# Performance work log

Measured on AMD Instinct MI355X. Metric: run time of the kernel, lower is better.

Reference implementation:

```python
import jax, jax.numpy as jnp
import numpy as np

EPS = 1e-5

def _layernorm(x, g, b):
    m = jnp.mean(x, axis=-1, keepdims=True)
    v = jnp.var(x, axis=-1, keepdims=True)
    return (x - m) * jax.lax.rsqrt(v + EPS) * g + b

def setup_inputs() -> dict:
    key = jax.random.key(0)
    ks = jax.random.split(key, 8)
    B, N, D, H = 4, 2048, 1024, 16
    F = 2 * D
    s = 0.02
    return {
        "x": jax.random.normal(ks[0], (B, N, D), jnp.float32),
        "mask": jnp.zeros((B, N, N), jnp.float32),
        "Wq": jax.random.normal(ks[1], (D, D), jnp.float32) * s,
        "Wk": jax.random.normal(ks[2], (D, D), jnp.float32) * s,
        "Wv": jax.random.normal(ks[3], (D, D), jnp.float32) * s,
        "Wc": jax.random.normal(ks[4], (D, D), jnp.float32) * s,
        "bc": jnp.zeros((D,), jnp.float32),
        "W1": jax.random.normal(ks[5], (D, F), jnp.float32) * s,
        "b1": jnp.zeros((F,), jnp.float32),
        "W2": jax.random.normal(ks[6], (F, D), jnp.float32) * s,
        "b2": jnp.zeros((D,), jnp.float32),
        "g1": jnp.ones((D,), jnp.float32),
        "be1": jnp.zeros((D,), jnp.float32),
        "g2": jnp.ones((D,), jnp.float32),
        "be2": jnp.zeros((D,), jnp.float32),
    }

def reference(x, mask, Wq, Wk, Wv, Wc, bc, W1, b1, W2, b2, g1, be1, g2, be2):
    B, N, D = x.shape
    H = 16
    Dh = D // H
    scale = 1.0 / np.sqrt(Dh).astype(np.float32)
    # projections -> [B, H, N, Dh]
    def heads(t):
        return t.reshape(B, N, H, Dh).transpose(0, 2, 1, 3)
    q = heads(x @ Wq)
    k = heads(x @ Wk)
    v = heads(x @ Wv)
    score = jnp.einsum('bhnd,bhmd->bhnm', q, k) * scale + mask[:, None, :, :]
    attn = jnp.einsum('bhnm,bhmd->bhnd', jax.nn.softmax(score, axis=-1), v)
    attn = attn.transpose(0, 2, 1, 3).reshape(B, N, D)
    x = x + attn @ Wc + bc
    x = _layernorm(x, g1, be1)
    x = x + jnp.maximum(x @ W1 + b1, 0.0) @ W2 + b2
    x = _layernorm(x, g2, be2)
    return x
```

## Files before the change

### kernel.cpp

```cpp
#include <hip/hip_runtime.h>
#include <hip/hip_bf16.h>


#define DEV __device__ __forceinline__

using s16x8 = __attribute__((ext_vector_type(8))) short;
using f32x4 = __attribute__((ext_vector_type(4))) float;

DEV unsigned short f2bf(float f) {
  unsigned u = __float_as_uint(f);
  u += 0x7fffu + ((u >> 16) & 1u);
  return (unsigned short)(u >> 16);
}
DEV unsigned pack2bf(float a, float b) {
  return (unsigned)f2bf(a) | ((unsigned)f2bf(b) << 16);
}
DEV unsigned cvt_pk_bf16(float lo, float hi) {
  unsigned r;
  asm("v_cvt_pk_bf16_f32 %0, %1, %2" : "=v"(r) : "v"(lo), "v"(hi));
  return r;
}

typedef __attribute__((address_space(3))) unsigned lds_u32_t;
typedef const __attribute__((address_space(1))) unsigned glb_u32_t;

DEV void gld_lds16(const void* g, void* l) {
  __builtin_amdgcn_global_load_lds((glb_u32_t*)g, (lds_u32_t*)l, 16, 0, 0);
}

template<int RELU, int RESID, int OUTF>
__global__ __launch_bounds__(256)
void gemm_bt(const unsigned short* __restrict__ A, const unsigned short* __restrict__ Bt,
             unsigned short* __restrict__ Cb, float* __restrict__ Cf,
             const float* __restrict__ bias, const float* __restrict__ resid,
             int M, int N, int K)
{
  __shared__ unsigned short As[128 * 32];
  __shared__ unsigned short Bs[128 * 32];
  const int tid  = threadIdx.x;
  const int wave = tid >> 6, lane = tid & 63;
  const int g = lane >> 4, q = lane & 15;

  const int nwg  = gridDim.x * gridDim.y;
  const int flat = blockIdx.y * gridDim.x + blockIdx.x;
  const int rm   = (nwg & 7) ? flat : ((flat & 7) * (nwg >> 3) + (flat >> 3));
  const int m0 = (rm / gridDim.x) * 128, n0 = (rm % gridDim.x) * 128;
  const int wr = wave >> 1, wc = wave & 1;

  f32x4 acc[4][4] = {};

  const int i0 = wave * 512 + lane * 8;
  const int i1 = 2048 + i0;

  for (int kt = 0; kt < K; kt += 32) {
    gld_lds16(A  + (size_t)(m0 + (i0 >> 5)) * K + kt + (i0 & 31), As + wave * 512);
    gld_lds16(Bt + (size_t)(n0 + (i0 >> 5)) * K + kt + (i0 & 31), Bs + wave * 512);
    gld_lds16(A  + (size_t)(m0 + (i1 >> 5)) * K + kt + (i1 & 31), As + 2048 + wave * 512);
    gld_lds16(Bt + (size_t)(n0 + (i1 >> 5)) * K + kt + (i1 & 31), Bs + 2048 + wave * 512);
    __syncthreads();
    s16x8 a[4], b[4];
#pragma unroll
    for (int m = 0; m < 4; ++m)
      a[m] = *(const s16x8*)(As + (wr * 64 + m * 16 + q) * 32 + g * 8);
#pragma unroll
    for (int n = 0; n < 4; ++n)
      b[n] = *(const s16x8*)(Bs + (wc * 64 + n * 16 + q) * 32 + g * 8);
#pragma unroll
    for (int m = 0; m < 4; ++m)
#pragma unroll
      for (int n = 0; n < 4; ++n)
        acc[m][n] = __builtin_amdgcn_mfma_f32_16x16x32_bf16(a[m], b[n], acc[m][n], 0, 0, 0);
    __syncthreads();
  }

#pragma unroll
  for (int n = 0; n < 4; ++n) {
    const int col = n0 + wc * 64 + n * 16 + q;
    const float bv = bias ? bias[col] : 0.0f;
#pragma unroll
    for (int m = 0; m < 4; ++m) {
      const int row0 = m0 + wr * 64 + m * 16 + g * 4;
#pragma unroll
      for (int r = 0; r < 4; ++r) {
        float v = acc[m][n][r] + bv;
        if (RELU) v = fmaxf(v, 0.0f);
        if (RESID) v += resid[(size_t)(row0 + r) * N + col];
        if (OUTF) Cf[(size_t)(row0 + r) * N + col] = v;
        else      Cb[(size_t)(row0 + r) * N + col] = f2bf(v);
      }
    }
  }
}

__global__ __launch_bounds__(256, 4)
void attn_kernel(const unsigned short* __restrict__ qkv,
                 const unsigned short* __restrict__ vt,
                 const float* __restrict__ mask,
                 unsigned short* __restrict__ outb)
{
  __shared__ unsigned short Ks[2][4096];
  __shared__ unsigned short Vs[2][4096];
  __shared__ unsigned short Pl[4][1024];
  const int tid = threadIdx.x, wave = tid >> 6, lane = tid & 63;
  const int g = lane >> 4, q = lane & 15;

  const int flat = blockIdx.y * 32 + blockIdx.x;
  const int rm   = (flat & 7) * 256 + (flat >> 3);
  const int qt = rm & 31, bh = rm >> 5;
  const int b = bh >> 4, h = bh & 15;
  const int qrow = qt * 64 + wave * 16;
  const size_t tok0 = (size_t)b * 2048;

  const unsigned short* Qp = qkv + (tok0 + qrow + q) * 3072 + h * 64;
  const s16x8 bq0 = *(const s16x8*)(Qp + g * 8);
  const s16x8 bq1 = *(const s16x8*)(Qp + 32 + g * 8);
  const float* Mp = mask + ((size_t)b * 2048 + qrow + q) * 2048;

  const int lr = lane >> 3;
  const int sc = (lane & 7) ^ lr;
  const unsigned short* Kg = qkv + tok0 * 3072 + 1024 + h * 64
                           + (size_t)(wave * 16 + lr) * 3072 + sc * 8;
  const unsigned short* Vg = vt + ((size_t)bh * 64 + wave * 16 + lr) * 2048 + sc * 8;
  unsigned short* KsW = Ks[0] + wave * 1024;
  unsigned short* VsW = Vs[0] + wave * 1024;

  auto STAGE = [&](int buf, int t) {
    const size_t ko = (size_t)t * (64 * 3072);
    const int    vo = t * 64;
    gld_lds16(Kg + ko,            KsW + buf * 4096);
    gld_lds16(Kg + ko + 8 * 3072, KsW + buf * 4096 + 512);
    gld_lds16(Vg + vo,            VsW + buf * 4096);
    gld_lds16(Vg + vo + 8 * 2048, VsW + buf * 4096 + 512);
  };

  f32x4 ot[4] = {};
  f32x4 mkc[4], mkn[4];
  float mrun = -3.0e38f, lsum = 0.0f;
  char* Pw = (char*)&Pl[wave][0];

  STAGE(0, 0);
#pragma unroll
  for (int m2 = 0; m2 < 4; ++m2) mkc[m2] = *(const f32x4*)(Mp + m2 * 16 + g * 4);
  __syncthreads();

  int cur = 0;
  for (int t = 0; t < 32; ++t) {
    if (t < 31) {
      STAGE(cur ^ 1, t + 1);
#pragma unroll
      for (int m2 = 0; m2 < 4; ++m2)
        mkn[m2] = *(const f32x4*)(Mp + (t + 1) * 64 + m2 * 16 + g * 4);
    }
    const unsigned short* Kt = Ks[cur];
    const unsigned short* Vt = Vs[cur];

    f32x4 st[4] = {};
    __builtin_amdgcn_s_setprio(1);
#pragma unroll
    for (int m2 = 0; m2 < 4; ++m2) {
      const unsigned short* kp = Kt + (m2 * 16 + q) * 64;
      const s16x8 ak0 = *(const s16x8*)(kp + ((g       ^ (q & 7)) * 8));
      const s16x8 ak1 = *(const s16x8*)(kp + (((g + 4) ^ (q & 7)) * 8));
      st[m2] = __builtin_amdgcn_mfma_f32_16x16x32_bf16(ak0, bq0, st[m2], 0, 0, 0);
      st[m2] = __builtin_amdgcn_mfma_f32_16x16x32_bf16(ak1, bq1, st[m2], 0, 0, 0);
    }
    __builtin_amdgcn_s_setprio(0);

    float tmax = -3.0e38f;
#pragma unroll
    for (int m2 = 0; m2 < 4; ++m2) {
#pragma unroll
      for (int r = 0; r < 4; ++r) {
        st[m2][r] = st[m2][r] * 0.125f + mkc[m2][r];
        tmax = fmaxf(tmax, st[m2][r]);
      }
    }
    tmax = fmaxf(tmax, __shfl_xor(tmax, 16));
    tmax = fmaxf(tmax, __shfl_xor(tmax, 32));
    const float mnew  = fmaxf(mrun, tmax);
    const float alpha = __expf(mrun - mnew);
    mrun = mnew;

    float rsum = 0.0f;
#pragma unroll
    for (int m2 = 0; m2 < 4; ++m2) {
#pragma unroll
      for (int r = 0; r < 4; ++r) {
        st[m2][r] = __expf(st[m2][r] - mnew);
        rsum += st[m2][r];
      }
      const int bir  = m2 * 32 + g * 8;
      const int addr = q * 128 + ((((bir >> 4) ^ (q & 7))) << 4) + (bir & 15);
      uint2 pk;
      pk.x = cvt_pk_bf16(st[m2][0], st[m2][1]);
      pk.y = cvt_pk_bf16(st[m2][2], st[m2][3]);
      *(uint2*)(Pw + addr) = pk;
    }
    rsum += __shfl_xor(rsum, 16);
    rsum += __shfl_xor(rsum, 32);
    lsum = lsum * alpha + rsum;
#pragma unroll
    for (int m = 0; m < 4; ++m) {
      ot[m][0] *= alpha; ot[m][1] *= alpha; ot[m][2] *= alpha; ot[m][3] *= alpha;
    }

    __builtin_amdgcn_s_setprio(1);
#pragma unroll
    for (int kb = 0; kb < 2; ++kb) {
      const int blk = (kb * 4 + g) ^ (q & 7);
      const s16x8 pb = *(const s16x8*)(Pw + q * 128 + blk * 16);
#pragma unroll
      for (int m = 0; m < 4; ++m) {
        const s16x8 av = *(const s16x8*)(Vt + (m * 16 + q) * 64 + blk * 8);
        ot[m] = __builtin_amdgcn_mfma_f32_16x16x32_bf16(av, pb, ot[m], 0, 0, 0);
      }
    }
    __builtin_amdgcn_s_setprio(0);

#pragma unroll
    for (int m2 = 0; m2 < 4; ++m2) mkc[m2] = mkn[m2];
    __syncthreads();
    cur ^= 1;
  }

  const float inv = 1.0f / lsum;
#pragma unroll
  for (int m = 0; m < 4; ++m) {
    const int bir  = m * 32 + g * 8;
    const int addr = q * 128 + (((bir >> 4) ^ (q & 7)) << 4) + (bir & 15);
    uint2 pk;
    pk.x = cvt_pk_bf16(ot[m][0] * inv, ot[m][1] * inv);
    pk.y = cvt_pk_bf16(ot[m][2] * inv, ot[m][3] * inv);
    *(uint2*)(Pw + addr) = pk;
  }
#pragma unroll
  for (int p = 0; p < 2; ++p) {
    const int c  = p * 64 + lane;
    const int qq = c >> 3, cc = c & 7;
    const int blk = cc ^ (qq & 7);
    const s16x8 vv = *(const s16x8*)(Pw + qq * 128 + blk * 16);
    *(s16x8*)(outb + (tok0 + qrow + qq) * 1024 + h * 64 + cc * 8) = vv;
  }
}

__global__ __launch_bounds__(256)
void ln_kernel(const float* __restrict__ in, float* __restrict__ outf,
               unsigned short* __restrict__ outb,
               const float* __restrict__ gam, const float* __restrict__ bet)
{
  __shared__ float red[8];
  const int row = blockIdx.x, tid = threadIdx.x;
  const f32x4 v = *(const f32x4*)(in + (size_t)row * 1024 + tid * 4);
  float s  = v[0] + v[1] + v[2] + v[3];
  float ss = v[0]*v[0] + v[1]*v[1] + v[2]*v[2] + v[3]*v[3];
#pragma unroll
  for (int o = 1; o < 64; o <<= 1) { s += __shfl_xor(s, o); ss += __shfl_xor(ss, o); }
  if ((tid & 63) == 0) { red[tid >> 6] = s; red[4 + (tid >> 6)] = ss; }
  __syncthreads();
  s  = red[0] + red[1] + red[2] + red[3];
  ss = red[4] + red[5] + red[6] + red[7];
  const float mean = s * (1.0f / 1024.0f);
  const float var  = ss * (1.0f / 1024.0f) - mean * mean;
  const float rstd = rsqrtf(var + 1e-5f);
  const f32x4 gm = *(const f32x4*)(gam + tid * 4);
  const f32x4 bt = *(const f32x4*)(bet + tid * 4);
  f32x4 o;
#pragma unroll
  for (int j = 0; j < 4; ++j) o[j] = (v[j] - mean) * rstd * gm[j] + bt[j];
  if (outf) *(f32x4*)(outf + (size_t)row * 1024 + tid * 4) = o;
  if (outb) {
    uint2 pk; pk.x = pack2bf(o[0], o[1]); pk.y = pack2bf(o[2], o[3]);
    *(uint2*)(outb + (size_t)row * 1024 + tid * 4) = pk;
  }
}

__global__ __launch_bounds__(256)
void tcast_kernel(const float* __restrict__ in, unsigned short* __restrict__ out, int R, int C)
{
  __shared__ float t[32][33];
  const int tx = threadIdx.x & 31, ty = threadIdx.x >> 5;
  const int c0 = blockIdx.x * 32, r0 = blockIdx.y * 32;
#pragma unroll
  for (int k = 0; k < 4; ++k)
    t[ty + k * 8][tx] = in[(size_t)(r0 + ty + k * 8) * C + c0 + tx];
  __syncthreads();
#pragma unroll
  for (int k = 0; k < 4; ++k)
    out[(size_t)(c0 + ty + k * 8) * R + r0 + tx] = f2bf(t[tx][ty + k * 8]);
}

__global__ __launch_bounds__(256)
void tv_kernel(const unsigned short* __restrict__ qkv, unsigned short* __restrict__ vt)
{
  __shared__ unsigned short t[32][33];
  const int tx = threadIdx.x & 31, ty = threadIdx.x >> 5;
  const int c0 = blockIdx.x * 32, r0 = blockIdx.y * 32, b = blockIdx.z;
  const unsigned short* in = qkv + (size_t)b * 2048 * 3072 + 2048;
  unsigned short* out = vt + (size_t)b * 1024 * 2048;
#pragma unroll
  for (int k = 0; k < 4; ++k)
    t[ty + k * 8][tx] = in[(size_t)(r0 + ty + k * 8) * 3072 + c0 + tx];
  __syncthreads();
#pragma unroll
  for (int k = 0; k < 4; ++k)
    out[(size_t)(c0 + ty + k * 8) * 2048 + r0 + tx] = t[tx][ty + k * 8];
}

__global__ __launch_bounds__(256)
void cast_x_kernel(const float* __restrict__ in, unsigned short* __restrict__ out)
{
  const size_t i = ((size_t)blockIdx.x * 256 + threadIdx.x) * 4;
  const f32x4 v = *(const f32x4*)(in + i);
  uint2 pk; pk.x = pack2bf(v[0], v[1]); pk.y = pack2bf(v[2], v[3]);
  *(uint2*)(out + i) = pk;
}

extern "C" void kernel_launch(void* const* d_in, const int* in_sizes, int n_in,
                              void* d_out, int out_size, void* d_ws, size_t ws_size,
                              hipStream_t stream)
{
  (void)in_sizes; (void)n_in; (void)out_size; (void)ws_size;
  const float* x   = (const float*)d_in[0];
  const float* msk = (const float*)d_in[1];
  const float* Wq  = (const float*)d_in[2];
  const float* Wk  = (const float*)d_in[3];
  const float* Wv  = (const float*)d_in[4];
  const float* Wc  = (const float*)d_in[5];
  const float* bc  = (const float*)d_in[6];
  const float* W1  = (const float*)d_in[7];
  const float* b1  = (const float*)d_in[8];
  const float* W2  = (const float*)d_in[9];
  const float* b2  = (const float*)d_in[10];
  const float* g1  = (const float*)d_in[11];
  const float* be1 = (const float*)d_in[12];
  const float* g2  = (const float*)d_in[13];
  const float* be2 = (const float*)d_in[14];
  float* out = (float*)d_out;
  char* ws = (char*)d_ws;
  const size_t MB = 1u << 20;
  unsigned short* xb    = (unsigned short*)(ws + 0 * MB);
  unsigned short* wqkvt = (unsigned short*)(ws + 16 * MB);
  unsigned short* wct   = (unsigned short*)(ws + 22 * MB);
  unsigned short* w1t   = (unsigned short*)(ws + 24 * MB);
  unsigned short* w2t   = (unsigned short*)(ws + 28 * MB);
  unsigned short* qkv   = (unsigned short*)(ws + 32 * MB);
  unsigned short* vt    = (unsigned short*)(ws + 80 * MB);
  unsigned short* attnb = xb;
  float*          y1    = (float*)(ws + 32 * MB);
  unsigned short* h1b   = (unsigned short*)(ws + 64 * MB);
  float*          h1f   = (float*)(ws + 96 * MB);
  unsigned short* midb  = (unsigned short*)(ws + 128 * MB);

  cast_x_kernel<<<8192, 256, 0, stream>>>(x, xb);
  tcast_kernel<<<dim3(32, 32), 256, 0, stream>>>(Wq, wqkvt,               1024, 1024);
  tcast_kernel<<<dim3(32, 32), 256, 0, stream>>>(Wk, wqkvt + 1024 * 1024, 1024, 1024);
  tcast_kernel<<<dim3(32, 32), 256, 0, stream>>>(Wv, wqkvt + 2048 * 1024, 1024, 1024);
  tcast_kernel<<<dim3(32, 32), 256, 0, stream>>>(Wc, wct,                 1024, 1024);
  tcast_kernel<<<dim3(64, 32), 256, 0, stream>>>(W1, w1t,                 1024, 2048);
  tcast_kernel<<<dim3(32, 64), 256, 0, stream>>>(W2, w2t,                 2048, 1024);

  gemm_bt<0, 0, 0><<<dim3(24, 64), 256, 0, stream>>>(xb, wqkvt, qkv, nullptr,
                                                     nullptr, nullptr, 8192, 3072, 1024);
  tv_kernel<<<dim3(32, 64, 4), 256, 0, stream>>>(qkv, vt);
  attn_kernel<<<dim3(32, 64), 256, 0, stream>>>(qkv, vt, msk, attnb);
  gemm_bt<0, 1, 1><<<dim3(8, 64), 256, 0, stream>>>(attnb, wct, nullptr, y1,
                                                    bc, x, 8192, 1024, 1024);
  ln_kernel<<<8192, 256, 0, stream>>>(y1, h1f, h1b, g1, be1);
  gemm_bt<1, 0, 0><<<dim3(16, 64), 256, 0, stream>>>(h1b, w1t, midb, nullptr,
                                                     b1, nullptr, 8192, 2048, 1024);
  gemm_bt<0, 1, 1><<<dim3(8, 64), 256, 0, stream>>>(midb, w2t, nullptr, out,
                                                    b2, h1f, 8192, 1024, 2048);
  ln_kernel<<<8192, 256, 0, stream>>>(out, out, nullptr, g2, be2);
}
```

Baseline: 470.6 us.

## Fuse V transpose into QKV GEMM and double attention query rows per wave

The QKV GEMM epilogue now writes the V columns directly in transposed layout, so the separate tv_kernel launch and its extra pass over V go away. The attention kernel processes 32 query rows per wave (128 per block), so each K/V tile staged in LDS is reused twice as often. Grid size is halved and occupancy is lowered to 3 blocks. Softmax switches to exp2 with a lazy rescale that only updates the running max when the new max exceeds it by more than 8. Mask prefetch across iterations is dropped in favour of in-iteration loads, and register pressure rises.

```diff
diff --git a/kernel.cpp b/kernel.cpp
--- a/kernel.cpp
+++ b/kernel.cpp
@@ -20,6 +20,12 @@
   asm("v_cvt_pk_bf16_f32 %0, %1, %2" : "=v"(r) : "v"(lo), "v"(hi));
   return r;
 }
+DEV f32x4 vmax4(f32x4 a, f32x4 b) {
+  f32x4 r;
+  r[0] = fmaxf(a[0], b[0]); r[1] = fmaxf(a[1], b[1]);
+  r[2] = fmaxf(a[2], b[2]); r[3] = fmaxf(a[3], b[3]);
+  return r;
+}
 
 typedef __attribute__((address_space(3))) unsigned lds_u32_t;
 typedef const __attribute__((address_space(1))) unsigned glb_u32_t;
@@ -28,11 +34,12 @@
   __builtin_amdgcn_global_load_lds((glb_u32_t*)g, (lds_u32_t*)l, 16, 0, 0);
 }
 
-template<int RELU, int RESID, int OUTF>
+template<int RELU, int RESID, int OUTF, int VOUT>
 __global__ __launch_bounds__(256)
 void gemm_bt(const unsigned short* __restrict__ A, const unsigned short* __restrict__ Bt,
              unsigned short* __restrict__ Cb, float* __restrict__ Cf,
              const float* __restrict__ bias, const float* __restrict__ resid,
+             unsigned short* __restrict__ vtout,
              int M, int N, int K)
 {
   __shared__ unsigned short As[128 * 32];
@@ -76,23 +83,36 @@
 #pragma unroll
   for (int n = 0; n < 4; ++n) {
     const int col = n0 + wc * 64 + n * 16 + q;
-    const float bv = bias ? bias[col] : 0.0f;
-#pragma unroll
-    for (int m = 0; m < 4; ++m) {
-      const int row0 = m0 + wr * 64 + m * 16 + g * 4;
-#pragma unroll
-      for (int r = 0; r < 4; ++r) {
-        float v = acc[m][n][r] + bv;
-        if (RELU) v = fmaxf(v, 0.0f);
-        if (RESID) v += resid[(size_t)(row0 + r) * N + col];
-        if (OUTF) Cf[(size_t)(row0 + r) * N + col] = v;
-        else      Cb[(size_t)(row0 + r) * N + col] = f2bf(v);
+    if (VOUT && col >= 2048) {
+      const int cv = col - 2048;
+#pragma unroll
+      for (int m = 0; m < 4; ++m) {
+        const int row0 = m0 + wr * 64 + m * 16 + g * 4;
+        const int bb = row0 >> 11;
+        ushort4 pk;
+        pk.x = f2bf(acc[m][n][0]); pk.y = f2bf(acc[m][n][1]);
+        pk.z = f2bf(acc[m][n][2]); pk.w = f2bf(acc[m][n][3]);
+        *(ushort4*)(vtout + ((size_t)bb * 1024 + cv) * 2048 + (row0 & 2047)) = pk;
       }
-    }
-  }
-}
-
-__global__ __launch_bounds__(256, 4)
+    } else {
+      const float bv = bias ? bias[col] : 0.0f;
+#pragma unroll
+      for (int m = 0; m < 4; ++m) {
+        const int row0 = m0 + wr * 64 + m * 16 + g * 4;
+#pragma unroll
+        for (int r = 0; r < 4; ++r) {
+          float v = acc[m][n][r] + bv;
+          if (RELU) v = fmaxf(v, 0.0f);
+          if (RESID) v += resid[(size_t)(row0 + r) * N + col];
+          if (OUTF) Cf[(size_t)(row0 + r) * N + col] = v;
+          else      Cb[(size_t)(row0 + r) * N + col] = f2bf(v);
+        }
+      }
+    }
+  }
+}
+
+__global__ __launch_bounds__(256, 3)
 void attn_kernel(const unsigned short* __restrict__ qkv,
                  const unsigned short* __restrict__ vt,
                  const float* __restrict__ mask,
@@ -100,21 +120,26 @@
 {
   __shared__ unsigned short Ks[2][4096];
   __shared__ unsigned short Vs[2][4096];
-  __shared__ unsigned short Pl[4][1024];
+  __shared__ unsigned short Pl[4][2048];
   const int tid = threadIdx.x, wave = tid >> 6, lane = tid & 63;
   const int g = lane >> 4, q = lane & 15;
 
-  const int flat = blockIdx.y * 32 + blockIdx.x;
-  const int rm   = (flat & 7) * 256 + (flat >> 3);
-  const int qt = rm & 31, bh = rm >> 5;
+  const int flat = blockIdx.y * 16 + blockIdx.x;
+  const int rm   = (flat & 7) * 128 + (flat >> 3);
+  const int qt = rm & 15, bh = rm >> 4;
   const int b = bh >> 4, h = bh & 15;
-  const int qrow = qt * 64 + wave * 16;
+  const int qrow = qt * 128 + wave * 32;
   const size_t tok0 = (size_t)b * 2048;
 
-  const unsigned short* Qp = qkv + (tok0 + qrow + q) * 3072 + h * 64;
-  const s16x8 bq0 = *(const s16x8*)(Qp + g * 8);
-  const s16x8 bq1 = *(const s16x8*)(Qp + 32 + g * 8);
-  const float* Mp = mask + ((size_t)b * 2048 + qrow + q) * 2048;
+  s16x8 bq[2][2];
+#pragma unroll
+  for (int qb = 0; qb < 2; ++qb) {
+    const unsigned short* Qp = qkv + (tok0 + qrow + qb * 16 + q) * 3072 + h * 64;
+    bq[qb][0] = *(const s16x8*)(Qp + g * 8);
+    bq[qb][1] = *(const s16x8*)(Qp + 32 + g * 8);
+  }
+  const float* Mp0 = mask + ((size_t)b * 2048 + qrow + q) * 2048;
+  const float* Mp1 = Mp0 + 16 * 2048;
 
   const int lr = lane >> 3;
   const int sc = (lane & 7) ^ lr;
@@ -133,108 +158,132 @@
     gld_lds16(Vg + vo + 8 * 2048, VsW + buf * 4096 + 512);
   };
 
-  f32x4 ot[4] = {};
-  f32x4 mkc[4], mkn[4];
-  float mrun = -3.0e38f, lsum = 0.0f;
+  f32x4 ot[2][4] = {};
+  float mrun0 = -3.0e38f, mrun1 = -3.0e38f;
+  float mnl0 = 0.0f, mnl1 = 0.0f;
+  float lsum0 = 0.0f, lsum1 = 0.0f;
   char* Pw = (char*)&Pl[wave][0];
+  const float SC  = 0.125f;
+  const float L2E = 1.4426950408889634f;
 
   STAGE(0, 0);
-#pragma unroll
-  for (int m2 = 0; m2 < 4; ++m2) mkc[m2] = *(const f32x4*)(Mp + m2 * 16 + g * 4);
   __syncthreads();
 
   int cur = 0;
+#pragma unroll 1
   for (int t = 0; t < 32; ++t) {
-    if (t < 31) {
-      STAGE(cur ^ 1, t + 1);
-#pragma unroll
-      for (int m2 = 0; m2 < 4; ++m2)
-        mkn[m2] = *(const f32x4*)(Mp + (t + 1) * 64 + m2 * 16 + g * 4);
+    if (t < 31) STAGE(cur ^ 1, t + 1);
+    f32x4 mk0[4], mk1[4];
+#pragma unroll
+    for (int m2 = 0; m2 < 4; ++m2) {
+      mk0[m2] = *(const f32x4*)(Mp0 + t * 64 + m2 * 16 + g * 4);
+      mk1[m2] = *(const f32x4*)(Mp1 + t * 64 + m2 * 16 + g * 4);
     }
     const unsigned short* Kt = Ks[cur];
     const unsigned short* Vt = Vs[cur];
 
-    f32x4 st[4] = {};
+    f32x4 st0[4] = {}, st1[4] = {};
     __builtin_amdgcn_s_setprio(1);
 #pragma unroll
     for (int m2 = 0; m2 < 4; ++m2) {
       const unsigned short* kp = Kt + (m2 * 16 + q) * 64;
       const s16x8 ak0 = *(const s16x8*)(kp + ((g       ^ (q & 7)) * 8));
       const s16x8 ak1 = *(const s16x8*)(kp + (((g + 4) ^ (q & 7)) * 8));
-      st[m2] = __builtin_amdgcn_mfma_f32_16x16x32_bf16(ak0, bq0, st[m2], 0, 0, 0);
-      st[m2] = __builtin_amdgcn_mfma_f32_16x16x32_bf16(ak1, bq1, st[m2], 0, 0, 0);
+      st0[m2] = __builtin_amdgcn_mfma_f32_16x16x32_bf16(ak0, bq[0][0], st0[m2], 0, 0, 0);
+      st1[m2] = __builtin_amdgcn_mfma_f32_16x16x32_bf16(ak0, bq[1][0], st1[m2], 0, 0, 0);
+      st0[m2] = __builtin_amdgcn_mfma_f32_16x16x32_bf16(ak1, bq[0][1], st0[m2], 0, 0, 0);
+      st1[m2] = __builtin_amdgcn_mfma_f32_16x16x32_bf16(ak1, bq[1][1], st1[m2], 0, 0, 0);
     }
     __builtin_amdgcn_s_setprio(0);
 
-    float tmax = -3.0e38f;
 #pragma unroll
     for (int m2 = 0; m2 < 4; ++m2) {
 #pragma unroll
       for (int r = 0; r < 4; ++r) {
-        st[m2][r] = st[m2][r] * 0.125f + mkc[m2][r];
-        tmax = fmaxf(tmax, st[m2][r]);
+        st0[m2][r] = fmaf(st0[m2][r], SC, mk0[m2][r]);
+        st1[m2][r] = fmaf(st1[m2][r], SC, mk1[m2][r]);
       }
     }
-    tmax = fmaxf(tmax, __shfl_xor(tmax, 16));
-    tmax = fmaxf(tmax, __shfl_xor(tmax, 32));
-    const float mnew  = fmaxf(mrun, tmax);
-    const float alpha = __expf(mrun - mnew);
-    mrun = mnew;
-
-    float rsum = 0.0f;
+    f32x4 a0 = vmax4(vmax4(st0[0], st0[1]), vmax4(st0[2], st0[3]));
+    f32x4 a1 = vmax4(vmax4(st1[0], st1[1]), vmax4(st1[2], st1[3]));
+    float t0 = fmaxf(fmaxf(a0[0], a0[1]), fmaxf(a0[2], a0[3]));
+    float t1 = fmaxf(fmaxf(a1[0], a1[1]), fmaxf(a1[2], a1[3]));
+    t0 = fmaxf(t0, __shfl_xor(t0, 16));
+    t0 = fmaxf(t0, __shfl_xor(t0, 32));
+    t1 = fmaxf(t1, __shfl_xor(t1, 16));
+    t1 = fmaxf(t1, __shfl_xor(t1, 32));
+
+    if (!__all(t0 <= mrun0 + 8.0f && t1 <= mrun1 + 8.0f)) {
+      const float mn0 = fmaxf(mrun0, t0), mn1 = fmaxf(mrun1, t1);
+      const float al0 = exp2f((mrun0 - mn0) * L2E);
+      const float al1 = exp2f((mrun1 - mn1) * L2E);
+      mrun0 = mn0; mrun1 = mn1;
+      mnl0 = mn0 * L2E; mnl1 = mn1 * L2E;
+      lsum0 *= al0; lsum1 *= al1;
+#pragma unroll
+      for (int m = 0; m < 4; ++m)
+#pragma unroll
+        for (int r = 0; r < 4; ++r) { ot[0][m][r] *= al0; ot[1][m][r] *= al1; }
+    }
+
+    float rs0 = 0.0f, rs1 = 0.0f;
 #pragma unroll
     for (int m2 = 0; m2 < 4; ++m2) {
 #pragma unroll
       for (int r = 0; r < 4; ++r) {
-        st[m2][r] = __expf(st[m2][r] - mnew);
-        rsum += st[m2][r];
+        st0[m2][r] = exp2f(fmaf(st0[m2][r], L2E, -mnl0));
+        st1[m2][r] = exp2f(fmaf(st1[m2][r], L2E, -mnl1));
       }
-      const int bir  = m2 * 32 + g * 8;
-      const int addr = q * 128 + ((((bir >> 4) ^ (q & 7))) << 4) + (bir & 15);
-      uint2 pk;
-      pk.x = cvt_pk_bf16(st[m2][0], st[m2][1]);
-      pk.y = cvt_pk_bf16(st[m2][2], st[m2][3]);
-      *(uint2*)(Pw + addr) = pk;
-    }
-    rsum += __shfl_xor(rsum, 16);
-    rsum += __shfl_xor(rsum, 32);
-    lsum = lsum * alpha + rsum;
-#pragma unroll
-    for (int m = 0; m < 4; ++m) {
-      ot[m][0] *= alpha; ot[m][1] *= alpha; ot[m][2] *= alpha; ot[m][3] *= alpha;
-    }
+      rs0 += (st0[m2][0] + st0[m2][1]) + (st0[m2][2] + st0[m2][3]);
+      rs1 += (st1[m2][0] + st1[m2][1]) + (st1[m2][2] + st1[m2][3]);
+      const int bir = m2 * 32 + g * 8;
+      const int ca  = (((bir >> 4) ^ (q & 7)) << 4) + (bir & 15);
+      uint2 pk0, pk1;
+      pk0.x = cvt_pk_bf16(st0[m2][0], st0[m2][1]);
+      pk0.y = cvt_pk_bf16(st0[m2][2], st0[m2][3]);
+      pk1.x = cvt_pk_bf16(st1[m2][0], st1[m2][1]);
+      pk1.y = cvt_pk_bf16(st1[m2][2], st1[m2][3]);
+      *(uint2*)(Pw + q * 128 + ca)        = pk0;
+      *(uint2*)(Pw + (16 + q) * 128 + ca) = pk1;
+    }
+    rs0 += __shfl_xor(rs0, 16); rs0 += __shfl_xor(rs0, 32);
+    rs1 += __shfl_xor(rs1, 16); rs1 += __shfl_xor(rs1, 32);
+    lsum0 += rs0; lsum1 += rs1;
 
     __builtin_amdgcn_s_setprio(1);
 #pragma unroll
     for (int kb = 0; kb < 2; ++kb) {
       const int blk = (kb * 4 + g) ^ (q & 7);
-      const s16x8 pb = *(const s16x8*)(Pw + q * 128 + blk * 16);
+      const s16x8 pb0 = *(const s16x8*)(Pw + q * 128 + blk * 16);
+      const s16x8 pb1 = *(const s16x8*)(Pw + (16 + q) * 128 + blk * 16);
 #pragma unroll
       for (int m = 0; m < 4; ++m) {
         const s16x8 av = *(const s16x8*)(Vt + (m * 16 + q) * 64 + blk * 8);
-        ot[m] = __builtin_amdgcn_mfma_f32_16x16x32_bf16(av, pb, ot[m], 0, 0, 0);
+        ot[0][m] = __builtin_amdgcn_mfma_f32_16x16x32_bf16(av, pb0, ot[0][m], 0, 0, 0);
+        ot[1][m] = __builtin_amdgcn_mfma_f32_16x16x32_bf16(av, pb1, ot[1][m], 0, 0, 0);
       }
     }
     __builtin_amdgcn_s_setprio(0);
 
-#pragma unroll
-    for (int m2 = 0; m2 < 4; ++m2) mkc[m2] = mkn[m2];
     __syncthreads();
     cur ^= 1;
   }
 
-  const float inv = 1.0f / lsum;
+  const float inv0 = 1.0f / lsum0, inv1 = 1.0f / lsum1;
 #pragma unroll
   for (int m = 0; m < 4; ++m) {
-    const int bir  = m * 32 + g * 8;
-    const int addr = q * 128 + (((bir >> 4) ^ (q & 7)) << 4) + (bir & 15);
-    uint2 pk;
-    pk.x = cvt_pk_bf16(ot[m][0] * inv, ot[m][1] * inv);
-    pk.y = cvt_pk_bf16(ot[m][2] * inv, ot[m][3] * inv);
-    *(uint2*)(Pw + addr) = pk;
-  }
-#pragma unroll
-  for (int p = 0; p < 2; ++p) {
+    const int bir = m * 32 + g * 8;
+    const int ca  = (((bir >> 4) ^ (q & 7)) << 4) + (bir & 15);
+    uint2 pk0, pk1;
+    pk0.x = cvt_pk_bf16(ot[0][m][0] * inv0, ot[0][m][1] * inv0);
+    pk0.y = cvt_pk_bf16(ot[0][m][2] * inv0, ot[0][m][3] * inv0);
+    pk1.x = cvt_pk_bf16(ot[1][m][0] * inv1, ot[1][m][1] * inv1);
+    pk1.y = cvt_pk_bf16(ot[1][m][2] * inv1, ot[1][m][3] * inv1);
+    *(uint2*)(Pw + q * 128 + ca)        = pk0;
+    *(uint2*)(Pw + (16 + q) * 128 + ca) = pk1;
+  }
+#pragma unroll
+  for (int p = 0; p < 4; ++p) {
     const int c  = p * 64 + lane;
     const int qq = c >> 3, cc = c & 7;
     const int blk = cc ^ (qq & 7);
@@ -287,23 +336,6 @@
 #pragma unroll
   for (int k = 0; k < 4; ++k)
     out[(size_t)(c0 + ty + k * 8) * R + r0 + tx] = f2bf(t[tx][ty + k * 8]);
-}
-
-__global__ __launch_bounds__(256)
-void tv_kernel(const unsigned short* __restrict__ qkv, unsigned short* __restrict__ vt)
-{
-  __shared__ unsigned short t[32][33];
-  const int tx = threadIdx.x & 31, ty = threadIdx.x >> 5;
-  const int c0 = blockIdx.x * 32, r0 = blockIdx.y * 32, b = blockIdx.z;
-  const unsigned short* in = qkv + (size_t)b * 2048 * 3072 + 2048;
-  unsigned short* out = vt + (size_t)b * 1024 * 2048;
-#pragma unroll
-  for (int k = 0; k < 4; ++k)
-    t[ty + k * 8][tx] = in[(size_t)(r0 + ty + k * 8) * 3072 + c0 + tx];
-  __syncthreads();
-#pragma unroll
-  for (int k = 0; k < 4; ++k)
-    out[(size_t)(c0 + ty + k * 8) * 2048 + r0 + tx] = t[tx][ty + k * 8];
 }
 
 __global__ __launch_bounds__(256)
@@ -359,16 +391,15 @@
   tcast_kernel<<<dim3(64, 32), 256, 0, stream>>>(W1, w1t,                 1024, 2048);
   tcast_kernel<<<dim3(32, 64), 256, 0, stream>>>(W2, w2t,                 2048, 1024);
 
-  gemm_bt<0, 0, 0><<<dim3(24, 64), 256, 0, stream>>>(xb, wqkvt, qkv, nullptr,
-                                                     nullptr, nullptr, 8192, 3072, 1024);
-  tv_kernel<<<dim3(32, 64, 4), 256, 0, stream>>>(qkv, vt);
-  attn_kernel<<<dim3(32, 64), 256, 0, stream>>>(qkv, vt, msk, attnb);
-  gemm_bt<0, 1, 1><<<dim3(8, 64), 256, 0, stream>>>(attnb, wct, nullptr, y1,
-                                                    bc, x, 8192, 1024, 1024);
+  gemm_bt<0, 0, 0, 1><<<dim3(24, 64), 256, 0, stream>>>(xb, wqkvt, qkv, nullptr,
+                                                        nullptr, nullptr, vt, 8192, 3072, 1024);
+  attn_kernel<<<dim3(16, 64), 256, 0, stream>>>(qkv, vt, msk, attnb);
+  gemm_bt<0, 1, 1, 0><<<dim3(8, 64), 256, 0, stream>>>(attnb, wct, nullptr, y1,
+                                                       bc, x, nullptr, 8192, 1024, 1024);
   ln_kernel<<<8192, 256, 0, stream>>>(y1, h1f, h1b, g1, be1);
-  gemm_bt<1, 0, 0><<<dim3(16, 64), 256, 0, stream>>>(h1b, w1t, midb, nullptr,
-                                                     b1, nullptr, 8192, 2048, 1024);
-  gemm_bt<0, 1, 1><<<dim3(8, 64), 256, 0, stream>>>(midb, w2t, nullptr, out,
-                                                    b2, h1f, 8192, 1024, 2048);
+  gemm_bt<1, 0, 0, 0><<<dim3(16, 64), 256, 0, stream>>>(h1b, w1t, midb, nullptr,
+                                                        b1, nullptr, nullptr, 8192, 2048, 1024);
+  gemm_bt<0, 1, 1, 0><<<dim3(8, 64), 256, 0, stream>>>(midb, w2t, nullptr, out,
+                                                       b2, h1f, nullptr, 8192, 1024, 2048);
   ln_kernel<<<8192, 256, 0, stream>>>(out, out, nullptr, g2, be2);
 }
```

Result: no change. 478.8 us (+1.8%).
